# Kernel tuning notes

Hardware: AMD Instinct MI355X
Metric: run time of the kernel (lower is better)

The kernel has to match this reference:

```python
import jax, jax.numpy as jnp
import numpy as np

# Static graph layout: B equal-size graphs so per-graph topk has a fixed size.
NUM_GRAPHS = 512
NODES_PER_GRAPH = 256
K_PER_GRAPH = 128  # ceil(0.5 * NODES_PER_GRAPH), ratio = 0.5
NUM_EDGES = 4_194_304  # avg degree 32
D_FEAT = 128
D_EDGE = 16


def setup_inputs() -> dict:
    key = jax.random.key(0)
    k1, k2, k3, k4, k5, k6 = jax.random.split(key, 6)
    N = NUM_GRAPHS * NODES_PER_GRAPH
    x = jax.random.normal(k1, (N, D_FEAT), dtype=jnp.float32)
    # Edges are sampled within a graph (realistic PyG batched-graph structure).
    g = jax.random.randint(k2, (NUM_EDGES,), 0, NUM_GRAPHS)
    src = g * NODES_PER_GRAPH + jax.random.randint(k3, (NUM_EDGES,), 0, NODES_PER_GRAPH)
    dst = g * NODES_PER_GRAPH + jax.random.randint(k4, (NUM_EDGES,), 0, NODES_PER_GRAPH)
    edge_index = jnp.stack([src, dst]).astype(jnp.int32)
    edge_attr = jax.random.normal(k5, (NUM_EDGES, D_EDGE), dtype=jnp.float32)
    batch = jnp.repeat(jnp.arange(NUM_GRAPHS, dtype=jnp.int32), NODES_PER_GRAPH)
    W = jax.random.normal(k6, (D_FEAT,), dtype=jnp.float32) / np.sqrt(D_FEAT)
    b = jnp.zeros((1,), dtype=jnp.float32)
    return {"x": x, "edge_index": edge_index, "edge_attr": edge_attr,
            "batch": batch, "W": W, "b": b}


def reference(x, edge_index, edge_attr, batch, W, b):
    N, D = x.shape
    B, n, k = NUM_GRAPHS, NODES_PER_GRAPH, K_PER_GRAPH
    K = B * k

    # --- SelectSparse: linear scoring (Linear(in_channels, 1)) ---
    scores = x @ W + b[0]                      # [N]
    # Per-graph top-k (batch is sorted with equal-size graphs -> reshape).
    top_vals, top_idx = jax.lax.top_k(scores.reshape(B, n), k)  # [B, k]
    perm = (top_idx + (jnp.arange(B) * n)[:, None]).reshape(-1)  # [K] global ids
    w = top_vals.reshape(-1)                   # scores[perm], descending per graph

    # --- gather + scale selected node features ---
    x_out = x[perm] * w[:, None]               # [K, D]

    # --- FilterEdges: keep edges with both endpoints selected, remap ids ---
    node_map = jnp.full((N,), -1, dtype=jnp.int32).at[perm].set(
        jnp.arange(K, dtype=jnp.int32))
    new_src = node_map[edge_index[0]]
    new_dst = node_map[edge_index[1]]
    mask = (new_src >= 0) & (new_dst >= 0)
    # Stable-compaction of kept edges to the front; tail padded with -1 / 0
    # (fixed output shape in lieu of torch's dynamic-shape edge filtering).
    order = jnp.argsort(jnp.logical_not(mask), stable=True)
    kept = mask[order]
    new_ei = jnp.stack([new_src[order], new_dst[order]])
    new_ei = jnp.where(kept[None, :], new_ei, -1)   # [2, E]
    new_attr = jnp.where(kept[:, None], edge_attr[order], 0.0)  # [E, D_EDGE]
    new_batch = batch[perm]                    # [K]

    return x_out, new_ei, new_attr, new_batch, perm, w
```

## Files before the change

### kernel.cpp

```cpp
#include <hip/hip_runtime.h>

#define NGRAPH 512
#define NPG    256
#define KPG    128
#define NN     (NGRAPH * NPG)
#define KK     (NGRAPH * KPG)
#define NE     4194304
#define DF     128
#define DE     16

#define SBLK   256
#define EPB    1024
#define NTILE  (NE / EPB)

typedef float vf4 __attribute__((ext_vector_type(4)));
typedef int   vi4 __attribute__((ext_vector_type(4)));

#define OUT_X     0ull
#define OUT_EI    ((size_t)KK * DF)
#define OUT_ATTR  (OUT_EI + 2ull * NE)
#define OUT_BATCH (OUT_ATTR + (size_t)NE * DE)
#define OUT_PERM  (OUT_BATCH + KK)
#define OUT_W     (OUT_PERM + KK)

__global__ void __launch_bounds__(NPG)
topk_all_kernel(const float* __restrict__ x,
                const float* __restrict__ W,
                const float* __restrict__ b,
                int* __restrict__ node_map,
                unsigned* __restrict__ nkbits,
                float* __restrict__ out) {
    __shared__ float s[NPG];
    __shared__ int   sel[KPG];
    __shared__ float selw[KPG];
    int g = blockIdx.x, t = threadIdx.x;
    int wave = t >> 6, lane = t & 63;
    int l32 = t & 31, grp = t >> 5;
    float bias = b[0];

    float4 wv = ((const float4*)W)[l32];
    #pragma unroll 4
    for (int it = 0; it < NPG / 8; it++) {
        int r = it * 8 + grp;
        float4 xv = ((const float4*)(x + ((size_t)g * NPG + r) * DF))[l32];
        float sum = xv.x * wv.x + xv.y * wv.y + xv.z * wv.z + xv.w * wv.w;
        #pragma unroll
        for (int off = 16; off > 0; off >>= 1) sum += __shfl_down(sum, off, 32);
        if (l32 == 0) s[r] = sum + bias;
    }
    __syncthreads();
    float my = s[t];
    int rank = 0;
    #pragma unroll 8
    for (int j = 0; j < NPG; j++) {
        float o = s[j];
        rank += (o > my) || (o == my && j < t);
    }
    bool kept = rank < KPG;
    if (kept) {
        int node = g * NPG + t;
        int nid  = g * KPG + rank;
        node_map[node] = nid;
        sel[rank]  = t;
        selw[rank] = my;
        out[OUT_BATCH + nid] = (float)g;
        out[OUT_PERM + nid]  = (float)node;
        out[OUT_W + nid]     = my;
    }
    unsigned long long bal = __ballot(kept);
    if (lane == 0)  nkbits[g * 8 + wave * 2]     = (unsigned)bal;
    if (lane == 32) nkbits[g * 8 + wave * 2 + 1] = (unsigned)(bal >> 32);
    __syncthreads();
    #pragma unroll
    for (int it = 0; it < KPG / 8; it++) {
        int r = it * 8 + grp;
        int node = g * NPG + sel[r];
        float wvs = selw[r];
        const vf4* sp = (const vf4*)(x + (size_t)node * DF);
        vf4 v = sp[l32];
        v *= wvs;
        __builtin_nontemporal_store(v,
            (vf4*)(out + OUT_X + ((size_t)g * KPG + r) * DF) + l32);
    }
}

__global__ void __launch_bounds__(SBLK)
mapstage_kernel(const int* __restrict__ ei,
                const int* __restrict__ node_map,
                const unsigned* __restrict__ nkbits,
                unsigned* __restrict__ pk_ws,
                unsigned short* __restrict__ kl_ws,
                int* __restrict__ tilecounts) {
    int tile = blockIdx.x, t = threadIdx.x;
    int wave = t >> 6, lane = t & 63;
    __shared__ int wtot[4];

    int ebase = tile * EPB + t * 4;
    vi4 sv = __builtin_nontemporal_load((const vi4*)(ei + ebase));
    vi4 dv = __builtin_nontemporal_load((const vi4*)(ei + NE + ebase));
    #define KB(n) ((nkbits[(unsigned)(n) >> 5] >> ((unsigned)(n) & 31u)) & 1u)
    unsigned bits = (KB(sv.x) & KB(dv.x))
                  | ((KB(sv.y) & KB(dv.y)) << 1)
                  | ((KB(sv.z) & KB(dv.z)) << 2)
                  | ((KB(sv.w) & KB(dv.w)) << 3);
    #undef KB
    int c = __popc(bits);
    int inc = c;
    #pragma unroll
    for (int off = 1; off < 64; off <<= 1) {
        int u = __shfl_up(inc, off, 64);
        if (lane >= off) inc += u;
    }
    if (lane == 63) wtot[wave] = inc;
    __syncthreads();
    int wbase = 0;
    #pragma unroll
    for (int i = 0; i < 4; i++) if (i < wave) wbase += wtot[i];
    int pre = wbase + inc - c;

    if (bits) {
        int s4[4] = {sv.x, sv.y, sv.z, sv.w};
        int d4[4] = {dv.x, dv.y, dv.z, dv.w};
        #pragma unroll
        for (int j = 0; j < 4; j++) {
            if ((bits >> j) & 1u) {
                unsigned ns = (unsigned)node_map[s4[j]];
                unsigned nd = (unsigned)node_map[d4[j]];
                pk_ws[tile * EPB + pre] = (ns << 16) | nd;
                kl_ws[tile * EPB + pre] = (unsigned short)(t * 4 + j);
                pre++;
            }
        }
    }
    if (t == 0) tilecounts[tile] = wtot[0] + wtot[1] + wtot[2] + wtot[3];
}

__global__ void __launch_bounds__(SBLK)
scatter_kernel(const float* __restrict__ eattr,
               const unsigned* __restrict__ pk_ws,
               const unsigned short* __restrict__ kl_ws,
               const int* __restrict__ tilecounts,
               float* __restrict__ out) {
    int tile = blockIdx.x, t = threadIdx.x;
    int wave = t >> 6, lane = t & 63;
    __shared__ int warr[4];
    __shared__ int s_excl;

    int partial = 0;
    for (int i = t; i < tile; i += SBLK) partial += tilecounts[i];
    #pragma unroll
    for (int off = 32; off > 0; off >>= 1) partial += __shfl_down(partial, off, 64);
    if (lane == 0) warr[wave] = partial;
    __syncthreads();
    if (t == 0) s_excl = warr[0] + warr[1] + warr[2] + warr[3];
    __syncthreads();
    int excl = s_excl;
    int cnt  = tilecounts[tile];

    for (int j = t; j < cnt; j += SBLK) {
        unsigned p = pk_ws[tile * EPB + j];
        __builtin_nontemporal_store((float)(p >> 16),     &out[OUT_EI + excl + j]);
        __builtin_nontemporal_store((float)(p & 0xFFFFu), &out[OUT_EI + NE + excl + j]);
    }
    int sub = t & 3;
    for (int j = t >> 2; j < cnt; j += SBLK / 4) {
        int el = kl_ws[tile * EPB + j];
        const vf4* sp = (const vf4*)(eattr + ((size_t)tile * EPB + el) * DE);
        vf4 v = __builtin_nontemporal_load(sp + sub);
        vf4* dp = (vf4*)(out + OUT_ATTR + ((size_t)excl + j) * DE);
        __builtin_nontemporal_store(v, dp + sub);
    }
    int disc_excl = tile * EPB - excl;
    int disc = EPB - cnt;
    size_t tail_lo = (size_t)NE - disc_excl - disc;
    for (int i = t; i < disc; i += SBLK) {
        __builtin_nontemporal_store(-1.f, &out[OUT_EI + tail_lo + i]);
        __builtin_nontemporal_store(-1.f, &out[OUT_EI + NE + tail_lo + i]);
    }
    vf4* ap = (vf4*)(out + OUT_ATTR);
    vf4 z = (vf4){0.f, 0.f, 0.f, 0.f};
    for (int i = t; i < disc * 4; i += SBLK)
        __builtin_nontemporal_store(z, &ap[tail_lo * 4 + i]);
}

extern "C" void kernel_launch(void* const* d_in, const int* in_sizes, int n_in,
                              void* d_out, int out_size, void* d_ws, size_t ws_size,
                              hipStream_t stream) {
    const float* x     = (const float*)d_in[0];
    const int*   ei    = (const int*)d_in[1];
    const float* eattr = (const float*)d_in[2];
    const float* W     = (const float*)d_in[4];
    const float* b     = (const float*)d_in[5];
    float* out = (float*)d_out;

    int*            node_map   = (int*)d_ws;
    unsigned*       nkbits     = (unsigned*)(node_map + NN);
    int*            tilecounts = (int*)(nkbits + NN / 32);
    unsigned*       pk_ws      = (unsigned*)(tilecounts + NTILE);
    unsigned short* kl_ws      = (unsigned short*)(pk_ws + NE);

    topk_all_kernel<<<NGRAPH, NPG, 0, stream>>>(x, W, b, node_map, nkbits, out);
    mapstage_kernel<<<NTILE, SBLK, 0, stream>>>(ei, node_map, nkbits, pk_ws, kl_ws, tilecounts);
    scatter_kernel <<<NTILE, SBLK, 0, stream>>>(eattr, pk_ws, kl_ws, tilecounts, out);
}
```

Before: 151.2 us.

## Vectorize top-k rank counting and drop nontemporal hints on loads/stores

The per-node rank computation now reads shared scores as float4 and splits the greater-than count from the tie-break equality count. Separately, all nontemporal loads and stores in the top-k gather and edge scatter kernels become ordinary cached accesses. The rank change cuts LDS instructions. Dropping the nontemporal hints changes cache behaviour for the large streaming outputs, which could help or hurt write bandwidth.

```diff
diff --git a/kernel.cpp b/kernel.cpp
--- a/kernel.cpp
+++ b/kernel.cpp
@@ -30,7 +30,7 @@
                 int* __restrict__ node_map,
                 unsigned* __restrict__ nkbits,
                 float* __restrict__ out) {
-    __shared__ float s[NPG];
+    __shared__ __align__(16) float s[NPG];
     __shared__ int   sel[KPG];
     __shared__ float selw[KPG];
     int g = blockIdx.x, t = threadIdx.x;
@@ -50,12 +50,20 @@
     }
     __syncthreads();
     float my = s[t];
+    const float4* s4p = (const float4*)s;
     int rank = 0;
     #pragma unroll 8
-    for (int j = 0; j < NPG; j++) {
-        float o = s[j];
-        rank += (o > my) || (o == my && j < t);
-    }
+    for (int j4 = 0; j4 < NPG / 4; j4++) {
+        float4 o = s4p[j4];
+        rank += (o.x > my) + (o.y > my) + (o.z > my) + (o.w > my);
+    }
+    int t4 = t >> 2;
+    for (int j4 = 0; j4 < t4; j4++) {
+        float4 o = s4p[j4];
+        rank += (o.x == my) + (o.y == my) + (o.z == my) + (o.w == my);
+    }
+    for (int j = t4 * 4; j < t; j++) rank += (s[j] == my);
+
     bool kept = rank < KPG;
     if (kept) {
         int node = g * NPG + t;
@@ -76,11 +84,9 @@
         int r = it * 8 + grp;
         int node = g * NPG + sel[r];
         float wvs = selw[r];
-        const vf4* sp = (const vf4*)(x + (size_t)node * DF);
-        vf4 v = sp[l32];
-        v *= wvs;
-        __builtin_nontemporal_store(v,
-            (vf4*)(out + OUT_X + ((size_t)g * KPG + r) * DF) + l32);
+        float4 v = ((const float4*)(x + (size_t)node * DF))[l32];
+        v.x *= wvs; v.y *= wvs; v.z *= wvs; v.w *= wvs;
+        ((float4*)(out + OUT_X + ((size_t)g * KPG + r) * DF))[l32] = v;
     }
 }
 
@@ -159,28 +165,28 @@
 
     for (int j = t; j < cnt; j += SBLK) {
         unsigned p = pk_ws[tile * EPB + j];
-        __builtin_nontemporal_store((float)(p >> 16),     &out[OUT_EI + excl + j]);
-        __builtin_nontemporal_store((float)(p & 0xFFFFu), &out[OUT_EI + NE + excl + j]);
+        out[OUT_EI + excl + j]      = (float)(p >> 16);
+        out[OUT_EI + NE + excl + j] = (float)(p & 0xFFFFu);
     }
     int sub = t & 3;
     for (int j = t >> 2; j < cnt; j += SBLK / 4) {
         int el = kl_ws[tile * EPB + j];
         const vf4* sp = (const vf4*)(eattr + ((size_t)tile * EPB + el) * DE);
-        vf4 v = __builtin_nontemporal_load(sp + sub);
+        vf4 v = sp[sub];
         vf4* dp = (vf4*)(out + OUT_ATTR + ((size_t)excl + j) * DE);
-        __builtin_nontemporal_store(v, dp + sub);
+        dp[sub] = v;
     }
     int disc_excl = tile * EPB - excl;
     int disc = EPB - cnt;
     size_t tail_lo = (size_t)NE - disc_excl - disc;
     for (int i = t; i < disc; i += SBLK) {
-        __builtin_nontemporal_store(-1.f, &out[OUT_EI + tail_lo + i]);
-        __builtin_nontemporal_store(-1.f, &out[OUT_EI + NE + tail_lo + i]);
+        out[OUT_EI + tail_lo + i]      = -1.f;
+        out[OUT_EI + NE + tail_lo + i] = -1.f;
     }
     vf4* ap = (vf4*)(out + OUT_ATTR);
     vf4 z = (vf4){0.f, 0.f, 0.f, 0.f};
     for (int i = t; i < disc * 4; i += SBLK)
-        __builtin_nontemporal_store(z, &ap[tail_lo * 4 + i]);
+        ap[tail_lo * 4 + i] = z;
 }
 
 extern "C" void kernel_launch(void* const* d_in, const int* in_sizes, int n_in,
```

Result: slower. 168.5 us (+11.4%).

## Move discarded-edge tail fill into a separate contiguous grid-stride kernel

Applied to the files above, without the earlier changes.

Removes the per-tile tail-padding writes from the scatter kernel. The mapstage kernel now accumulates a global kept-edge total with an atomic, and a new kernel fills the whole tail with -1 and zeros using contiguous grid-stride stores. The top-k rank loop is also vectorized to read shared memory as float4, with the tie-break comparisons restricted to earlier indices. This adds a fourth launch and one atomic per tile, in exchange for replacing many small scattered tail segments with one coalesced streaming region.

```diff
diff --git a/kernel.cpp b/kernel.cpp
--- a/kernel.cpp
+++ b/kernel.cpp
@@ -29,14 +29,16 @@
                 const float* __restrict__ b,
                 int* __restrict__ node_map,
                 unsigned* __restrict__ nkbits,
+                int* __restrict__ d_total,
                 float* __restrict__ out) {
-    __shared__ float s[NPG];
+    __shared__ __align__(16) float s[NPG];
     __shared__ int   sel[KPG];
     __shared__ float selw[KPG];
     int g = blockIdx.x, t = threadIdx.x;
     int wave = t >> 6, lane = t & 63;
     int l32 = t & 31, grp = t >> 5;
     float bias = b[0];
+    if (g == 0 && t == 0) d_total[0] = 0;
 
     float4 wv = ((const float4*)W)[l32];
     #pragma unroll 4
@@ -50,12 +52,20 @@
     }
     __syncthreads();
     float my = s[t];
+    const float4* s4p = (const float4*)s;
     int rank = 0;
     #pragma unroll 8
-    for (int j = 0; j < NPG; j++) {
-        float o = s[j];
-        rank += (o > my) || (o == my && j < t);
-    }
+    for (int j4 = 0; j4 < NPG / 4; j4++) {
+        float4 o = s4p[j4];
+        rank += (o.x > my) + (o.y > my) + (o.z > my) + (o.w > my);
+    }
+    int t4 = t >> 2;
+    for (int j4 = 0; j4 < t4; j4++) {
+        float4 o = s4p[j4];
+        rank += (o.x == my) + (o.y == my) + (o.z == my) + (o.w == my);
+    }
+    for (int j = t4 * 4; j < t; j++) rank += (s[j] == my);
+
     bool kept = rank < KPG;
     if (kept) {
         int node = g * NPG + t;
@@ -90,7 +100,8 @@
                 const unsigned* __restrict__ nkbits,
                 unsigned* __restrict__ pk_ws,
                 unsigned short* __restrict__ kl_ws,
-                int* __restrict__ tilecounts) {
+                int* __restrict__ tilecounts,
+                int* __restrict__ d_total) {
     int tile = blockIdx.x, t = threadIdx.x;
     int wave = t >> 6, lane = t & 63;
     __shared__ int wtot[4];
@@ -132,7 +143,11 @@
             }
         }
     }
-    if (t == 0) tilecounts[tile] = wtot[0] + wtot[1] + wtot[2] + wtot[3];
+    if (t == 0) {
+        int cnt = wtot[0] + wtot[1] + wtot[2] + wtot[3];
+        tilecounts[tile] = cnt;
+        atomicAdd(d_total, cnt);
+    }
 }
 
 __global__ void __launch_bounds__(SBLK)
@@ -170,17 +185,22 @@
         vf4* dp = (vf4*)(out + OUT_ATTR + ((size_t)excl + j) * DE);
         __builtin_nontemporal_store(v, dp + sub);
     }
-    int disc_excl = tile * EPB - excl;
-    int disc = EPB - cnt;
-    size_t tail_lo = (size_t)NE - disc_excl - disc;
-    for (int i = t; i < disc; i += SBLK) {
-        __builtin_nontemporal_store(-1.f, &out[OUT_EI + tail_lo + i]);
-        __builtin_nontemporal_store(-1.f, &out[OUT_EI + NE + tail_lo + i]);
-    }
+}
+
+__global__ void __launch_bounds__(256)
+tailfill_kernel(const int* __restrict__ d_total,
+                float* __restrict__ out) {
+    int total = d_total[0];
+    size_t stride = (size_t)gridDim.x * blockDim.x;
+    size_t tid = (size_t)blockIdx.x * blockDim.x + threadIdx.x;
+    for (size_t i = (size_t)total + tid; i < NE; i += stride)
+        __builtin_nontemporal_store(-1.f, &out[OUT_EI + i]);
+    for (size_t i = (size_t)total + tid; i < NE; i += stride)
+        __builtin_nontemporal_store(-1.f, &out[OUT_EI + NE + i]);
     vf4* ap = (vf4*)(out + OUT_ATTR);
     vf4 z = (vf4){0.f, 0.f, 0.f, 0.f};
-    for (int i = t; i < disc * 4; i += SBLK)
-        __builtin_nontemporal_store(z, &ap[tail_lo * 4 + i]);
+    for (size_t i = (size_t)total * 4 + tid; i < (size_t)NE * 4; i += stride)
+        __builtin_nontemporal_store(z, &ap[i]);
 }
 
 extern "C" void kernel_launch(void* const* d_in, const int* in_sizes, int n_in,
@@ -196,10 +216,12 @@
     int*            node_map   = (int*)d_ws;
     unsigned*       nkbits     = (unsigned*)(node_map + NN);
     int*            tilecounts = (int*)(nkbits + NN / 32);
-    unsigned*       pk_ws      = (unsigned*)(tilecounts + NTILE);
+    int*            d_total    = tilecounts + NTILE;
+    unsigned*       pk_ws      = (unsigned*)(d_total + 64);
     unsigned short* kl_ws      = (unsigned short*)(pk_ws + NE);
 
-    topk_all_kernel<<<NGRAPH, NPG, 0, stream>>>(x, W, b, node_map, nkbits, out);
-    mapstage_kernel<<<NTILE, SBLK, 0, stream>>>(ei, node_map, nkbits, pk_ws, kl_ws, tilecounts);
+    topk_all_kernel<<<NGRAPH, NPG, 0, stream>>>(x, W, b, node_map, nkbits, d_total, out);
+    mapstage_kernel<<<NTILE, SBLK, 0, stream>>>(ei, node_map, nkbits, pk_ws, kl_ws, tilecounts, d_total);
     scatter_kernel <<<NTILE, SBLK, 0, stream>>>(eattr, pk_ws, kl_ws, tilecounts, out);
-}
+    tailfill_kernel<<<2048, 256, 0, stream>>>(d_total, out);
+}
```

New measurement: 184.1 us. 1.22x slower.
